# Kernel tuning notes

Hardware: AMD Instinct MI355X
Metric: run time of the kernel (lower is better)

The kernel has to match this reference:

```python
import jax, jax.numpy as jnp
import numpy as np

N_HEAD, M_DIM, K_DIM, V_DIM = 16, 1024, 64, 64
LN_EPS = 1e-5


def setup_inputs() -> dict:
    key = jax.random.key(0)
    ks = jax.random.split(key, 10)
    B, L = 4, 2048
    q = jax.random.normal(ks[0], (B, L, M_DIM), dtype=jnp.float32)
    k = jax.random.normal(ks[1], (B, L, M_DIM), dtype=jnp.float32)
    v = jax.random.normal(ks[2], (B, L, M_DIM), dtype=jnp.float32)
    s = 1.0 / np.sqrt(M_DIM)
    W_qs = jax.random.normal(ks[3], (M_DIM, N_HEAD * K_DIM), dtype=jnp.float32) * s
    W_ks = jax.random.normal(ks[4], (M_DIM, N_HEAD * K_DIM), dtype=jnp.float32) * s
    W_vs = jax.random.normal(ks[5], (M_DIM, N_HEAD * V_DIM), dtype=jnp.float32) * s
    fc_w = jax.random.normal(ks[6], (N_HEAD * V_DIM, M_DIM), dtype=jnp.float32) * (1.0 / np.sqrt(N_HEAD * V_DIM))
    fc_b = jnp.zeros((M_DIM,), dtype=jnp.float32)
    ln_g = jnp.ones((M_DIM,), dtype=jnp.float32)
    ln_b = jnp.zeros((M_DIM,), dtype=jnp.float32)
    return {"q": q, "k": k, "v": v, "W_qs": W_qs, "W_ks": W_ks, "W_vs": W_vs,
            "fc_w": fc_w, "fc_b": fc_b, "ln_g": ln_g, "ln_b": ln_b}


def reference(q, k, v, W_qs, W_ks, W_vs, fc_w, fc_b, ln_g, ln_b):
    B, Lq, _ = q.shape
    residual = q
    # project and split heads: [B, L, H, D]
    qh = (q @ W_qs).reshape(B, Lq, N_HEAD, K_DIM)
    kh = (k @ W_ks).reshape(B, k.shape[1], N_HEAD, K_DIM)
    vh = (v @ W_vs).reshape(B, v.shape[1], N_HEAD, V_DIM)
    temperature = np.power(K_DIM, 0.5).astype(np.float32)
    # attention scores [B, H, Lq, Lk]
    attn = jnp.einsum('bqhd,bkhd->bhqk', qh, kh) / temperature
    attn = jax.nn.softmax(attn, axis=-1)
    out = jnp.einsum('bhqk,bkhd->bqhd', attn, vh).reshape(B, Lq, N_HEAD * V_DIM)
    out = out @ fc_w + fc_b
    x = out + residual
    mu = jnp.mean(x, axis=-1, keepdims=True)
    var = jnp.mean(jnp.square(x - mu), axis=-1, keepdims=True)
    return (x - mu) * jax.lax.rsqrt(var + LN_EPS) * ln_g + ln_b
```

## Files before the change

kernel.cpp:

```cpp
#include <hip/hip_runtime.h>
#include <math.h>

#define NHEAD 16
#define MDIM  1024
#define KD    64
#define BATCH 4
#define SEQ   2048
#define MROWS (BATCH*SEQ)

using short8 = __attribute__((ext_vector_type(8))) short;
using f4     = __attribute__((ext_vector_type(4))) float;
using f16x   = __attribute__((ext_vector_type(16))) float;

__device__ inline short f2bf(float x) {
  union { float f; unsigned u; } v; v.f = x;
  unsigned r = v.u + 0x7fffu + ((v.u >> 16) & 1u);
  return (short)(r >> 16);
}

__device__ __forceinline__ float fast_exp2(float x) {
#if __has_builtin(__builtin_amdgcn_exp2f)
  return __builtin_amdgcn_exp2f(x);
#else
  return exp2f(x);
#endif
}

__device__ __forceinline__ int pack_bf16(float lo, float hi) {
#if __has_builtin(__builtin_amdgcn_cvt_pk_bf16_f32)
  auto t = __builtin_amdgcn_cvt_pk_bf16_f32(lo, hi);
  int r; __builtin_memcpy(&r, &t, 4); return r;
#else
  unsigned u0 = __float_as_uint(lo) + 0x8000u;
  unsigned u1 = __float_as_uint(hi) + 0x8000u;
  return (int)__builtin_amdgcn_perm(u1, u0, 0x07060302u);
#endif
}

__device__ __forceinline__ void g2l16(const void* g, void* l) {
  __builtin_amdgcn_global_load_lds((const __attribute__((address_space(1))) unsigned int*)g,
                                   (__attribute__((address_space(3))) unsigned int*)l, 16, 0, 0);
}

#define AHIP_WAIT_LGKM0 asm volatile("s_waitcnt lgkmcnt(0)" ::: "memory")
#define AHIP_WAIT_VM4   asm volatile("s_waitcnt vmcnt(4)" ::: "memory")
#define AHIP_WAIT_VM0   asm volatile("s_waitcnt vmcnt(0)" ::: "memory")
#define AHIP_SFENCE     __builtin_amdgcn_sched_barrier(0)
#define AHIP_BAR        __builtin_amdgcn_s_barrier()

__global__ void wtrans_kernel(const float* __restrict__ w0, const float* __restrict__ w1,
                              const float* __restrict__ w2, const float* __restrict__ w3,
                              short* __restrict__ o0, short* __restrict__ o1,
                              short* __restrict__ o2, short* __restrict__ o3) {
  int z = blockIdx.z;
  const float* in = z == 0 ? w0 : (z == 1 ? w1 : (z == 2 ? w2 : w3));
  short* out = z == 0 ? o0 : (z == 1 ? o1 : (z == 2 ? o2 : o3));
  __shared__ float t[32][33];
  int bx = blockIdx.x * 32, by = blockIdx.y * 32;
  int tx = threadIdx.x, ty = threadIdx.y;
#pragma unroll
  for (int i = 0; i < 4; i++)
    t[ty + i * 8][tx] = in[(size_t)(by + ty + i * 8) * MDIM + bx + tx];
  __syncthreads();
#pragma unroll
  for (int i = 0; i < 4; i++)
    out[(size_t)(bx + ty + i * 8) * MDIM + by + tx] = f2bf(t[tx][ty + i * 8]);
}

__global__ void cvt_kernel(const float* __restrict__ q, const float* __restrict__ k,
                           const float* __restrict__ v, short* __restrict__ qb,
                           short* __restrict__ kb, short* __restrict__ vb) {
  const float* in = blockIdx.y == 0 ? q : (blockIdx.y == 1 ? k : v);
  short* out = blockIdx.y == 0 ? qb : (blockIdx.y == 1 ? kb : vb);
  size_t i = (size_t)blockIdx.x * 256 + threadIdx.x;
  float4 a = ((const float4*)in)[2 * i];
  float4 b = ((const float4*)in)[2 * i + 1];
  short8 s = {f2bf(a.x), f2bf(a.y), f2bf(a.z), f2bf(a.w),
              f2bf(b.x), f2bf(b.y), f2bf(b.z), f2bf(b.w)};
  ((short8*)out)[i] = s;
}

#define G8_PROLOGUE(Ab, Bt)                                                            \
  int tid = threadIdx.x, wid = tid >> 6, lane = tid & 63;                              \
  int quad = lane >> 4, low = lane & 15;                                               \
  int l8 = lane & 7, lr = lane >> 3;                                                   \
  int wrow = (wid >> 2) * 64, wcol = (wid & 3) * 32;                                   \
  const short* aS = Ab + (size_t)(m0 + wid * 16 + lr) * 1024 + (l8 ^ lr) * 8;          \
  const short* bS = Bt + (size_t)(n0 + wid * 16 + lr) * 1024 + (l8 ^ lr) * 8;          \
  auto stage = [&](int t, int b) {                                                     \
    const short* a = aS + t * 64;                                                      \
    const short* bb = bS + t * 64;                                                     \
    short* ad = &As[b][wid * 1024];                                                    \
    short* bd = &Bs[b][wid * 1024];                                                    \
    g2l16(a, ad);                                                                      \
    g2l16(a + 8 * 1024, ad + 512);                                                     \
    g2l16(bb, bd);                                                                     \
    g2l16(bb + 8 * 1024, bd + 512);                                                    \
  };                                                                                   \
  f4 acc[4][2];                                                                        \
  _Pragma("unroll")                                                                    \
  for (int mf = 0; mf < 4; mf++)                                                       \
    _Pragma("unroll")                                                                  \
    for (int nf = 0; nf < 2; nf++) {                                                   \
      acc[mf][nf][0] = 0.f; acc[mf][nf][1] = 0.f;                                      \
      acc[mf][nf][2] = 0.f; acc[mf][nf][3] = 0.f;                                      \
    }                                                                                  \
  stage(0, 0);                                                                         \
  stage(1, 1);                                                                         \
  AHIP_WAIT_VM4; AHIP_SFENCE; AHIP_BAR; AHIP_SFENCE;

#define G8_MAIN_LOOP()                                                                 \
  for (int t = 0; t < 16; ++t) {                                                       \
    const int cur = t & 1;                                                             \
    short8 af[2][4], bfv[2][2];                                                        \
    _Pragma("unroll")                                                                  \
    for (int kk = 0; kk < 2; kk++) {                                                   \
      _Pragma("unroll")                                                                \
      for (int mf = 0; mf < 4; mf++)                                                   \
        af[kk][mf] = *(const short8*)&As[cur][(wrow + mf * 16 + low) * 64 +            \
                                              (((kk * 4 + quad) ^ (low & 7)) * 8)];    \
      _Pragma("unroll")                                                                \
      for (int nf = 0; nf < 2; nf++)                                                   \
        bfv[kk][nf] = *(const short8*)&Bs[cur][(wcol + nf * 16 + low) * 64 +           \
                                               (((kk * 4 + quad) ^ (low & 7)) * 8)];   \
    }                                                                                  \
    AHIP_WAIT_LGKM0; AHIP_SFENCE;                                                      \
    AHIP_BAR; AHIP_SFENCE;                                                             \
    if (t + 2 < 16) stage(t + 2, cur);                                                 \
    __builtin_amdgcn_s_setprio(1);                                                     \
    _Pragma("unroll")                                                                  \
    for (int kk = 0; kk < 2; kk++)                                                     \
      _Pragma("unroll")                                                                \
      for (int mf = 0; mf < 4; mf++)                                                   \
        _Pragma("unroll")                                                              \
        for (int nf = 0; nf < 2; nf++)                                                 \
          acc[mf][nf] = __builtin_amdgcn_mfma_f32_16x16x32_bf16(af[kk][mf],            \
                          bfv[kk][nf], acc[mf][nf], 0, 0, 0);                          \
    __builtin_amdgcn_s_setprio(0);                                                     \
    AHIP_SFENCE;                                                                       \
    if (t + 2 < 16) { AHIP_WAIT_VM4; } else { AHIP_WAIT_VM0; }                         \
    AHIP_SFENCE; AHIP_BAR; AHIP_SFENCE;                                                \
  }

__launch_bounds__(512, 4)
__global__ void gemm_qkv_kernel(const short* __restrict__ qb, const short* __restrict__ kb,
                                const short* __restrict__ vb, const short* __restrict__ Wqt,
                                const short* __restrict__ Wkt, const short* __restrict__ Wvt,
                                short* __restrict__ Qh, short* __restrict__ Kh,
                                short* __restrict__ Vt) {
  __shared__ __attribute__((aligned(16))) short As[2][128 * 64];
  __shared__ __attribute__((aligned(16))) short Bs[2][128 * 64];
  int z = blockIdx.z;
  const short* Ab = z == 0 ? qb : (z == 1 ? kb : vb);
  const short* Bt = z == 0 ? Wqt : (z == 1 ? Wkt : Wvt);
  int m0 = blockIdx.x * 128, n0 = blockIdx.y * 128;

  G8_PROLOGUE(Ab, Bt)
  G8_MAIN_LOOP()

  float scale = z == 0 ? 0.18033688011112042f : 1.0f;
  short* dst = z == 0 ? Qh : (z == 1 ? Kh : Vt);
#pragma unroll
  for (int mf = 0; mf < 4; mf++)
#pragma unroll
    for (int nf = 0; nf < 2; nf++)
#pragma unroll
      for (int r2 = 0; r2 < 4; r2++) {
        int gr = m0 + wrow + mf * 16 + quad * 4 + r2;
        int gc = n0 + wcol + nf * 16 + low;
        float val = acc[mf][nf][r2];
        int b = gr >> 11, l = gr & 2047, h = gc >> 6, d = gc & 63;
        if (z < 2)
          dst[(((size_t)(b * NHEAD + h)) * SEQ + l) * KD + d] = f2bf(val * scale);
        else
          dst[(((size_t)(b * NHEAD + h)) * KD + d) * SEQ + l] = f2bf(val);
      }
}

__launch_bounds__(512, 4)
__global__ void gemm_fc_kernel(const short* __restrict__ Ab, const short* __restrict__ Bt,
                               float* __restrict__ dst, const float* __restrict__ bias,
                               const float* __restrict__ res) {
  __shared__ __attribute__((aligned(16))) short As[2][128 * 64];
  __shared__ __attribute__((aligned(16))) short Bs[2][128 * 64];
  int m0 = blockIdx.x * 128, n0 = blockIdx.y * 128;

  G8_PROLOGUE(Ab, Bt)
  G8_MAIN_LOOP()

#pragma unroll
  for (int mf = 0; mf < 4; mf++)
#pragma unroll
    for (int nf = 0; nf < 2; nf++)
#pragma unroll
      for (int r2 = 0; r2 < 4; r2++) {
        int gr = m0 + wrow + mf * 16 + quad * 4 + r2;
        int gc = n0 + wcol + nf * 16 + low;
        dst[(size_t)gr * 1024 + gc] = acc[mf][nf][r2] + bias[gc] + res[(size_t)gr * 1024 + gc];
      }
}

__launch_bounds__(128, 2)
__global__ void attn_kernel(const short* __restrict__ Qh, const short* __restrict__ Kh,
                            const short* __restrict__ Vt, short* __restrict__ Out) {
  __shared__ __attribute__((aligned(16))) short KT[2][64 * 64];
  __shared__ __attribute__((aligned(16))) short VT[2][64 * 64];
  int tid = threadIdx.x;
  int wave = tid >> 6, lane = tid & 63;
  int l = lane & 31, hi = lane >> 5;
  int bh = blockIdx.y;
  int q0 = blockIdx.x * 128 + wave * 64;

  const short* Qb = Qh + (size_t)bh * SEQ * KD;
  const short* Kb = Kh + (size_t)bh * SEQ * KD;
  const short* Vb = Vt + (size_t)bh * KD * SEQ;

  int srow = lane >> 3;
  int sch = (lane & 7) ^ srow;
  const short* kS = Kb + (size_t)(wave * 32 + srow) * KD + sch * 8;
  const short* vS = Vb + (size_t)(wave * 32 + srow) * SEQ + sch * 8;

  auto stage = [&](int k0, int b) {
    short* kd = &KT[b][wave * 2048];
    short* vd = &VT[b][wave * 2048];
#pragma unroll
    for (int i = 0; i < 4; i++) {
      g2l16(kS + (size_t)(k0 + i * 8) * KD, kd + i * 512);
      g2l16(vS + (size_t)(i * 8) * SEQ + k0, vd + i * 512);
    }
  };

  short8 qf[2][4];
#pragma unroll
  for (int qt = 0; qt < 2; qt++)
#pragma unroll
    for (int ks = 0; ks < 4; ks++)
      qf[qt][ks] = *(const short8*)&Qb[(size_t)(q0 + qt * 32 + l) * KD + ks * 16 + hi * 8];

  f16x Oacc[2][2], lacc[2];
#pragma unroll
  for (int i = 0; i < 16; i++) {
    Oacc[0][0][i] = 0.f; Oacc[0][1][i] = 0.f;
    Oacc[1][0][i] = 0.f; Oacc[1][1][i] = 0.f;
    lacc[0][i] = 0.f; lacc[1][i] = 0.f;
  }
  f16x fz;
#pragma unroll
  for (int i = 0; i < 16; i++) fz[i] = 0.f;
  const short8 onesb = {0x3F80, 0x3F80, 0x3F80, 0x3F80, 0x3F80, 0x3F80, 0x3F80, 0x3F80};

  stage(0, 0);
  __syncthreads();

  for (int c = 0; c < SEQ / 64; c++) {
    int b = c & 1;
    if (c + 1 < SEQ / 64) stage((c + 1) * 64, b ^ 1);

#pragma unroll
    for (int nt = 0; nt < 2; nt++) {
      short8 kf[4];
#pragma unroll
      for (int ks = 0; ks < 4; ks++)
        kf[ks] = *(const short8*)&KT[b][(nt * 32 + l) * 64 + (((ks * 2 + hi) ^ (l & 7)) * 8)];
      short8 vf00 = *(const short8*)&VT[b][l * 64 + (((nt * 4 + 0 + hi) ^ (l & 7)) * 8)];
      short8 vf01 = *(const short8*)&VT[b][l * 64 + (((nt * 4 + 2 + hi) ^ (l & 7)) * 8)];
      short8 vf10 = *(const short8*)&VT[b][(32 + l) * 64 + (((nt * 4 + 0 + hi) ^ (l & 7)) * 8)];
      short8 vf11 = *(const short8*)&VT[b][(32 + l) * 64 + (((nt * 4 + 2 + hi) ^ (l & 7)) * 8)];

#pragma unroll
      for (int qt = 0; qt < 2; qt++) {
        f16x S;
        __builtin_amdgcn_s_setprio(1);
        S = __builtin_amdgcn_mfma_f32_32x32x16_bf16(kf[0], qf[qt][0], fz, 0, 0, 0);
        S = __builtin_amdgcn_mfma_f32_32x32x16_bf16(kf[1], qf[qt][1], S, 0, 0, 0);
        S = __builtin_amdgcn_mfma_f32_32x32x16_bf16(kf[2], qf[qt][2], S, 0, 0, 0);
        S = __builtin_amdgcn_mfma_f32_32x32x16_bf16(kf[3], qf[qt][3], S, 0, 0, 0);
        __builtin_amdgcn_s_setprio(0);

        int u[8];
#pragma unroll
        for (int i = 0; i < 8; i++)
          u[i] = pack_bf16(fast_exp2(S[2 * i]), fast_exp2(S[2 * i + 1]));
        asm("v_permlane32_swap_b32 %0, %1" : "+v"(u[0]), "+v"(u[2]));
        asm("v_permlane32_swap_b32 %0, %1" : "+v"(u[1]), "+v"(u[3]));
        asm("v_permlane32_swap_b32 %0, %1" : "+v"(u[4]), "+v"(u[6]));
        asm("v_permlane32_swap_b32 %0, %1" : "+v"(u[5]), "+v"(u[7]));
        short8 pa0, pa1;
        {
          int t0[4] = {u[0], u[1], u[2], u[3]};
          int t1[4] = {u[4], u[5], u[6], u[7]};
          __builtin_memcpy(&pa0, t0, 16);
          __builtin_memcpy(&pa1, t1, 16);
        }

        __builtin_amdgcn_s_setprio(1);
        lacc[qt] = __builtin_amdgcn_mfma_f32_32x32x16_bf16(pa0, onesb, lacc[qt], 0, 0, 0);
        lacc[qt] = __builtin_amdgcn_mfma_f32_32x32x16_bf16(pa1, onesb, lacc[qt], 0, 0, 0);
        Oacc[qt][0] = __builtin_amdgcn_mfma_f32_32x32x16_bf16(pa0, vf00, Oacc[qt][0], 0, 0, 0);
        Oacc[qt][0] = __builtin_amdgcn_mfma_f32_32x32x16_bf16(pa1, vf01, Oacc[qt][0], 0, 0, 0);
        Oacc[qt][1] = __builtin_amdgcn_mfma_f32_32x32x16_bf16(pa0, vf10, Oacc[qt][1], 0, 0, 0);
        Oacc[qt][1] = __builtin_amdgcn_mfma_f32_32x32x16_bf16(pa1, vf11, Oacc[qt][1], 0, 0, 0);
        __builtin_amdgcn_s_setprio(0);
      }
    }
    __syncthreads();
  }

  int bb = bh >> 4, h = bh & 15;
#pragma unroll
  for (int qt = 0; qt < 2; qt++)
#pragma unroll
    for (int r = 0; r < 16; r++) {
      int qrow = q0 + qt * 32 + (r & 3) + 8 * (r >> 2) + 4 * hi;
      float iv = 1.0f / lacc[qt][r];
#pragma unroll
      for (int dt = 0; dt < 2; dt++) {
        size_t idx = ((size_t)(bb * SEQ + qrow)) * 1024 + h * 64 + dt * 32 + l;
        Out[idx] = f2bf(Oacc[qt][dt][r] * iv);
      }
    }
}

__launch_bounds__(256)
__global__ void ln_kernel(const float* __restrict__ x, const float* __restrict__ g,
                          const float* __restrict__ b, float* __restrict__ out) {
  int row = blockIdx.x, tid = threadIdx.x;
  const float4* xr = (const float4*)(x + (size_t)row * 1024);
  float4 v = xr[tid];
  float s = v.x + v.y + v.z + v.w;
  float q = v.x * v.x + v.y * v.y + v.z * v.z + v.w * v.w;
#pragma unroll
  for (int o = 32; o > 0; o >>= 1) { s += __shfl_xor(s, o); q += __shfl_xor(q, o); }
  __shared__ float ss[4], sq[4];
  if ((tid & 63) == 0) { ss[tid >> 6] = s; sq[tid >> 6] = q; }
  __syncthreads();
  if (tid == 0) {
    float S = ss[0] + ss[1] + ss[2] + ss[3];
    float Q = sq[0] + sq[1] + sq[2] + sq[3];
    float mean = S * (1.f / 1024.f);
    float var = Q * (1.f / 1024.f) - mean * mean;
    ss[0] = mean; sq[0] = rsqrtf(var + 1e-5f);
  }
  __syncthreads();
  float mean = ss[0], rs = sq[0];
  const float4* g4 = (const float4*)g;
  const float4* b4 = (const float4*)b;
  float4 gg = g4[tid], bb = b4[tid], o;
  o.x = (v.x - mean) * rs * gg.x + bb.x;
  o.y = (v.y - mean) * rs * gg.y + bb.y;
  o.z = (v.z - mean) * rs * gg.z + bb.z;
  o.w = (v.w - mean) * rs * gg.w + bb.w;
  ((float4*)(out + (size_t)row * 1024))[tid] = o;
}

extern "C" void kernel_launch(void* const* d_in, const int* in_sizes, int n_in,
                              void* d_out, int out_size, void* d_ws, size_t ws_size,
                              hipStream_t stream) {
  const float* q   = (const float*)d_in[0];
  const float* k   = (const float*)d_in[1];
  const float* v   = (const float*)d_in[2];
  const float* Wq  = (const float*)d_in[3];
  const float* Wk  = (const float*)d_in[4];
  const float* Wv  = (const float*)d_in[5];
  const float* fcw = (const float*)d_in[6];
  const float* fcb = (const float*)d_in[7];
  const float* lng = (const float*)d_in[8];
  const float* lnb = (const float*)d_in[9];
  float* out = (float*)d_out;

  char* ws = (char*)d_ws;
  const size_t MB = 1024 * 1024;
  short* Wqt = (short*)(ws + 0 * MB);
  short* Wkt = (short*)(ws + 2 * MB);
  short* Wvt = (short*)(ws + 4 * MB);
  short* fct = (short*)(ws + 6 * MB);
  short* qb  = (short*)(ws + 8 * MB);
  short* kb  = (short*)(ws + 24 * MB);
  short* vb  = (short*)(ws + 40 * MB);
  short* Kh  = (short*)(ws + 8 * MB);
  short* Vt  = (short*)(ws + 24 * MB);
  short* Ao  = (short*)(ws + 40 * MB);
  short* Qh  = (short*)(ws + 56 * MB);
  float* X   = (float*)(ws + 8 * MB);

  wtrans_kernel<<<dim3(32, 32, 4), dim3(32, 8), 0, stream>>>(Wq, Wk, Wv, fcw, Wqt, Wkt, Wvt, fct);

  cvt_kernel<<<dim3(MROWS * MDIM / 8 / 256, 3), 256, 0, stream>>>(q, k, v, qb, kb, vb);

  gemm_qkv_kernel<<<dim3(64, 8, 3), 512, 0, stream>>>(qb, kb, vb, Wqt, Wkt, Wvt, Qh, Kh, Vt);

  attn_kernel<<<dim3(SEQ / 128, BATCH * NHEAD), 128, 0, stream>>>(Qh, Kh, Vt, Ao);

  gemm_fc_kernel<<<dim3(64, 8), 512, 0, stream>>>(Ao, fct, X, fcb, q);

  ln_kernel<<<MROWS, 256, 0, stream>>>(X, lng, lnb, out);
}
```

Measured before the change: 348.1 us.

## Use 8-wave attention blocks with 32 query rows per wave

The attention kernel now launches 512-thread blocks of 8 waves covering 256 queries, each wave owning 32 query rows instead of 64. K/V tile staging is split across 8 waves, one 16-byte load per wave per tensor, so each staged tile is shared by more query rows. Per-wave register use roughly halves, which should allow higher occupancy. In exchange, each K/V LDS fragment now feeds one QK MFMA chain instead of two, and V fragments are reloaded inside the loop, so LDS reads per unit of MFMA work go up.

After: 347.3 us. No clear change (-0.2%).

```diff
diff --git a/kernel.cpp b/kernel.cpp
--- a/kernel.cpp
+++ b/kernel.cpp
@@ -200,7 +200,7 @@
       }
 }
 
-__launch_bounds__(128, 2)
+__launch_bounds__(512, 4)
 __global__ void attn_kernel(const short* __restrict__ Qh, const short* __restrict__ Kh,
                             const short* __restrict__ Vt, short* __restrict__ Out) {
   __shared__ __attribute__((aligned(16))) short KT[2][64 * 64];
@@ -209,7 +209,7 @@
   int wave = tid >> 6, lane = tid & 63;
   int l = lane & 31, hi = lane >> 5;
   int bh = blockIdx.y;
-  int q0 = blockIdx.x * 128 + wave * 64;
+  int q0 = blockIdx.x * 256 + wave * 32;
 
   const short* Qb = Qh + (size_t)bh * SEQ * KD;
   const short* Kb = Kh + (size_t)bh * SEQ * KD;
@@ -217,36 +217,22 @@
 
   int srow = lane >> 3;
   int sch = (lane & 7) ^ srow;
-  const short* kS = Kb + (size_t)(wave * 32 + srow) * KD + sch * 8;
-  const short* vS = Vb + (size_t)(wave * 32 + srow) * SEQ + sch * 8;
+  const short* kS = Kb + (size_t)(wave * 8 + srow) * KD + sch * 8;
+  const short* vS = Vb + (size_t)(wave * 8 + srow) * SEQ + sch * 8;
 
   auto stage = [&](int k0, int b) {
-    short* kd = &KT[b][wave * 2048];
-    short* vd = &VT[b][wave * 2048];
-#pragma unroll
-    for (int i = 0; i < 4; i++) {
-      g2l16(kS + (size_t)(k0 + i * 8) * KD, kd + i * 512);
-      g2l16(vS + (size_t)(i * 8) * SEQ + k0, vd + i * 512);
-    }
+    g2l16(kS + (size_t)k0 * KD, &KT[b][wave * 512]);
+    g2l16(vS + k0, &VT[b][wave * 512]);
   };
 
-  short8 qf[2][4];
-#pragma unroll
-  for (int qt = 0; qt < 2; qt++)
-#pragma unroll
-    for (int ks = 0; ks < 4; ks++)
-      qf[qt][ks] = *(const short8*)&Qb[(size_t)(q0 + qt * 32 + l) * KD + ks * 16 + hi * 8];
-
-  f16x Oacc[2][2], lacc[2];
-#pragma unroll
-  for (int i = 0; i < 16; i++) {
-    Oacc[0][0][i] = 0.f; Oacc[0][1][i] = 0.f;
-    Oacc[1][0][i] = 0.f; Oacc[1][1][i] = 0.f;
-    lacc[0][i] = 0.f; lacc[1][i] = 0.f;
-  }
-  f16x fz;
-#pragma unroll
-  for (int i = 0; i < 16; i++) fz[i] = 0.f;
+  short8 qf[4];
+#pragma unroll
+  for (int ks = 0; ks < 4; ks++)
+    qf[ks] = *(const short8*)&Qb[(size_t)(q0 + l) * KD + ks * 16 + hi * 8];
+
+  f16x Oacc[2], lacc, fz;
+#pragma unroll
+  for (int i = 0; i < 16; i++) { Oacc[0][i] = 0.f; Oacc[1][i] = 0.f; lacc[i] = 0.f; fz[i] = 0.f; }
   const short8 onesb = {0x3F80, 0x3F80, 0x3F80, 0x3F80, 0x3F80, 0x3F80, 0x3F80, 0x3F80};
 
   stage(0, 0);
@@ -262,63 +248,58 @@
 #pragma unroll
       for (int ks = 0; ks < 4; ks++)
         kf[ks] = *(const short8*)&KT[b][(nt * 32 + l) * 64 + (((ks * 2 + hi) ^ (l & 7)) * 8)];
-      short8 vf00 = *(const short8*)&VT[b][l * 64 + (((nt * 4 + 0 + hi) ^ (l & 7)) * 8)];
-      short8 vf01 = *(const short8*)&VT[b][l * 64 + (((nt * 4 + 2 + hi) ^ (l & 7)) * 8)];
-      short8 vf10 = *(const short8*)&VT[b][(32 + l) * 64 + (((nt * 4 + 0 + hi) ^ (l & 7)) * 8)];
-      short8 vf11 = *(const short8*)&VT[b][(32 + l) * 64 + (((nt * 4 + 2 + hi) ^ (l & 7)) * 8)];
-
-#pragma unroll
-      for (int qt = 0; qt < 2; qt++) {
-        f16x S;
-        __builtin_amdgcn_s_setprio(1);
-        S = __builtin_amdgcn_mfma_f32_32x32x16_bf16(kf[0], qf[qt][0], fz, 0, 0, 0);
-        S = __builtin_amdgcn_mfma_f32_32x32x16_bf16(kf[1], qf[qt][1], S, 0, 0, 0);
-        S = __builtin_amdgcn_mfma_f32_32x32x16_bf16(kf[2], qf[qt][2], S, 0, 0, 0);
-        S = __builtin_amdgcn_mfma_f32_32x32x16_bf16(kf[3], qf[qt][3], S, 0, 0, 0);
-        __builtin_amdgcn_s_setprio(0);
-
-        int u[8];
-#pragma unroll
-        for (int i = 0; i < 8; i++)
-          u[i] = pack_bf16(fast_exp2(S[2 * i]), fast_exp2(S[2 * i + 1]));
-        asm("v_permlane32_swap_b32 %0, %1" : "+v"(u[0]), "+v"(u[2]));
-        asm("v_permlane32_swap_b32 %0, %1" : "+v"(u[1]), "+v"(u[3]));
-        asm("v_permlane32_swap_b32 %0, %1" : "+v"(u[4]), "+v"(u[6]));
-        asm("v_permlane32_swap_b32 %0, %1" : "+v"(u[5]), "+v"(u[7]));
-        short8 pa0, pa1;
-        {
-          int t0[4] = {u[0], u[1], u[2], u[3]};
-          int t1[4] = {u[4], u[5], u[6], u[7]};
-          __builtin_memcpy(&pa0, t0, 16);
-          __builtin_memcpy(&pa1, t1, 16);
-        }
-
-        __builtin_amdgcn_s_setprio(1);
-        lacc[qt] = __builtin_amdgcn_mfma_f32_32x32x16_bf16(pa0, onesb, lacc[qt], 0, 0, 0);
-        lacc[qt] = __builtin_amdgcn_mfma_f32_32x32x16_bf16(pa1, onesb, lacc[qt], 0, 0, 0);
-        Oacc[qt][0] = __builtin_amdgcn_mfma_f32_32x32x16_bf16(pa0, vf00, Oacc[qt][0], 0, 0, 0);
-        Oacc[qt][0] = __builtin_amdgcn_mfma_f32_32x32x16_bf16(pa1, vf01, Oacc[qt][0], 0, 0, 0);
-        Oacc[qt][1] = __builtin_amdgcn_mfma_f32_32x32x16_bf16(pa0, vf10, Oacc[qt][1], 0, 0, 0);
-        Oacc[qt][1] = __builtin_amdgcn_mfma_f32_32x32x16_bf16(pa1, vf11, Oacc[qt][1], 0, 0, 0);
-        __builtin_amdgcn_s_setprio(0);
+
+      f16x S;
+      __builtin_amdgcn_s_setprio(1);
+      S = __builtin_amdgcn_mfma_f32_32x32x16_bf16(kf[0], qf[0], fz, 0, 0, 0);
+      S = __builtin_amdgcn_mfma_f32_32x32x16_bf16(kf[1], qf[1], S, 0, 0, 0);
+      S = __builtin_amdgcn_mfma_f32_32x32x16_bf16(kf[2], qf[2], S, 0, 0, 0);
+      S = __builtin_amdgcn_mfma_f32_32x32x16_bf16(kf[3], qf[3], S, 0, 0, 0);
+      __builtin_amdgcn_s_setprio(0);
+
+      int u[8];
+#pragma unroll
+      for (int i = 0; i < 8; i++)
+        u[i] = pack_bf16(fast_exp2(S[2 * i]), fast_exp2(S[2 * i + 1]));
+      asm("v_permlane32_swap_b32 %0, %1" : "+v"(u[0]), "+v"(u[2]));
+      asm("v_permlane32_swap_b32 %0, %1" : "+v"(u[1]), "+v"(u[3]));
+      asm("v_permlane32_swap_b32 %0, %1" : "+v"(u[4]), "+v"(u[6]));
+      asm("v_permlane32_swap_b32 %0, %1" : "+v"(u[5]), "+v"(u[7]));
+      short8 pa0, pa1;
+      {
+        int t0[4] = {u[0], u[1], u[2], u[3]};
+        int t1[4] = {u[4], u[5], u[6], u[7]};
+        __builtin_memcpy(&pa0, t0, 16);
+        __builtin_memcpy(&pa1, t1, 16);
       }
+
+      __builtin_amdgcn_s_setprio(1);
+      lacc = __builtin_amdgcn_mfma_f32_32x32x16_bf16(pa0, onesb, lacc, 0, 0, 0);
+      lacc = __builtin_amdgcn_mfma_f32_32x32x16_bf16(pa1, onesb, lacc, 0, 0, 0);
+
+#pragma unroll
+      for (int dt = 0; dt < 2; dt++) {
+        short8 vf0 = *(const short8*)&VT[b][(dt * 32 + l) * 64 + (((nt * 4 + 0 + hi) ^ (l & 7)) * 8)];
+        short8 vf1 = *(const short8*)&VT[b][(dt * 32 + l) * 64 + (((nt * 4 + 2 + hi) ^ (l & 7)) * 8)];
+        Oacc[dt] = __builtin_amdgcn_mfma_f32_32x32x16_bf16(pa0, vf0, Oacc[dt], 0, 0, 0);
+        Oacc[dt] = __builtin_amdgcn_mfma_f32_32x32x16_bf16(pa1, vf1, Oacc[dt], 0, 0, 0);
+      }
+      __builtin_amdgcn_s_setprio(0);
     }
     __syncthreads();
   }
 
   int bb = bh >> 4, h = bh & 15;
 #pragma unroll
-  for (int qt = 0; qt < 2; qt++)
-#pragma unroll
-    for (int r = 0; r < 16; r++) {
-      int qrow = q0 + qt * 32 + (r & 3) + 8 * (r >> 2) + 4 * hi;
-      float iv = 1.0f / lacc[qt][r];
-#pragma unroll
-      for (int dt = 0; dt < 2; dt++) {
-        size_t idx = ((size_t)(bb * SEQ + qrow)) * 1024 + h * 64 + dt * 32 + l;
-        Out[idx] = f2bf(Oacc[qt][dt][r] * iv);
-      }
+  for (int r = 0; r < 16; r++) {
+    int qrow = q0 + (r & 3) + 8 * (r >> 2) + 4 * hi;
+    float iv = 1.0f / lacc[r];
+#pragma unroll
+    for (int dt = 0; dt < 2; dt++) {
+      size_t idx = ((size_t)(bb * SEQ + qrow)) * 1024 + h * 64 + dt * 32 + l;
+      Out[idx] = f2bf(Oacc[dt][r] * iv);
     }
+  }
 }
 
 __launch_bounds__(256)
@@ -389,7 +370,7 @@
 
   gemm_qkv_kernel<<<dim3(64, 8, 3), 512, 0, stream>>>(qb, kb, vb, Wqt, Wkt, Wvt, Qh, Kh, Vt);
 
-  attn_kernel<<<dim3(SEQ / 128, BATCH * NHEAD), 128, 0, stream>>>(Qh, Kh, Vt, Ao);
+  attn_kernel<<<dim3(SEQ / 256, BATCH * NHEAD), 512, 0, stream>>>(Qh, Kh, Vt, Ao);
 
   gemm_fc_kernel<<<dim3(64, 8), 512, 0, stream>>>(Ao, fct, X, fcb, q);
 
```
